# Kernel optimization log

Measured on AMD Instinct MI355X. Metric: run time of the kernel, lower is better.

Reference implementation:

```python
import jax, jax.numpy as jnp
import numpy as np

B, T, I, H = 256, 512, 300, 128


def setup_inputs() -> dict:
    key = jax.random.key(0)
    ks = jax.random.split(key, 7)
    s_ih = 1.0 / np.sqrt(H)
    return {
        "x": jax.random.normal(ks[0], (B, T, I), dtype=jnp.float32),
        # PyTorch LSTM params, gate order i,f,g,o stacked along first axis
        "W_ih": jax.random.uniform(ks[1], (4 * H, I), minval=-s_ih, maxval=s_ih, dtype=jnp.float32),
        "W_hh": jax.random.uniform(ks[2], (4 * H, H), minval=-s_ih, maxval=s_ih, dtype=jnp.float32),
        "b_ih": jax.random.uniform(ks[3], (4 * H,), minval=-s_ih, maxval=s_ih, dtype=jnp.float32),
        "b_hh": jax.random.uniform(ks[4], (4 * H,), minval=-s_ih, maxval=s_ih, dtype=jnp.float32),
        "fc_w": jax.random.uniform(ks[5], (1, H), minval=-s_ih, maxval=s_ih, dtype=jnp.float32),
        "fc_b": jax.random.uniform(ks[6], (1,), minval=-s_ih, maxval=s_ih, dtype=jnp.float32),
    }


def _lstm_last_h(x, W_ih, W_hh, b_ih, b_hh):
    # Precompute input contributions for all timesteps at once: [B,T,4H]
    xg = jnp.einsum("bti,gi->btg", x, W_ih) + b_ih + b_hh
    xg = jnp.transpose(xg, (1, 0, 2))  # [T,B,4H] for scan

    def step(carry, xg_t):
        h, c = carry
        gates = xg_t + h @ W_hh.T  # [B,4H]
        i, f, g, o = jnp.split(gates, 4, axis=-1)
        i = jax.nn.sigmoid(i)
        f = jax.nn.sigmoid(f)
        g = jnp.tanh(g)
        o = jax.nn.sigmoid(o)
        c = f * c + i * g
        h = o * jnp.tanh(c)
        return (h, c), None

    h0 = jnp.zeros((x.shape[0], W_hh.shape[1]), dtype=x.dtype)
    (h_last, _), _ = jax.lax.scan(step, (h0, h0), xg)
    return h_last  # [B,H]


def reference(x, W_ih, W_hh, b_ih, b_hh, fc_w, fc_b):
    h_last = _lstm_last_h(x, W_ih, W_hh, b_ih, b_hh)
    return h_last @ fc_w.T + fc_b  # [B,1]
```

## Files before the change

kernel.cpp:

```cpp
#include <hip/hip_runtime.h>
#include <cstdint>
#include <cstddef>

#define Bb   256
#define Tt   512
#define Ii   300
#define Hh   128
#define G4   512
#define KP   320
#define Mm   (Bb*Tt)

typedef _Float16 h2v   __attribute__((ext_vector_type(2)));
typedef _Float16 half8 __attribute__((ext_vector_type(8)));
typedef float    f32x4 __attribute__((ext_vector_type(4)));

static __device__ __forceinline__ h2v as_h2(unsigned int u){ union{unsigned int u; h2v h;} c; c.u=u; return c.h; }
static __device__ __forceinline__ unsigned int as_u32(h2v h){ union{unsigned int u; h2v h;} c; c.h=h; return c.u; }

#if __has_builtin(__builtin_amdgcn_fdot2)
#define FDOT2(a,b,c) __builtin_amdgcn_fdot2((a),(b),(c),false)
#else
static __device__ __forceinline__ float FDOT2(h2v a, h2v b, float c){
  return c + (float)a[0]*(float)b[0] + (float)a[1]*(float)b[1];
}
#endif

__global__ __launch_bounds__(256) void conv_x(const float* __restrict__ x, unsigned int* __restrict__ x16){
  int idx = blockIdx.x*256 + threadIdx.x;
  int r   = idx / 160;
  int kk2 = idx - r*160;
  int kk  = kk2*2;
  const float* xr = x + (size_t)r*Ii;
  float v0 = (kk   < Ii) ? xr[kk]   : 0.f;
  float v1 = (kk+1 < Ii) ? xr[kk+1] : 0.f;
  h2v h; h[0] = (_Float16)v0; h[1] = (_Float16)v1;
  x16[idx] = as_u32(h);
}

__global__ __launch_bounds__(256) void conv_small(const float* __restrict__ Wih, const float* __restrict__ Whh,
      const float* __restrict__ bih, const float* __restrict__ bhh,
      unsigned int* __restrict__ W16, unsigned int* __restrict__ Whh2, float* __restrict__ bias){
  int idx = blockIdx.x*256 + threadIdx.x;
  if (idx < G4*160){
    int pr = idx/160, kk2 = idx - pr*160, kk = kk2*2;
    int gc = (pr&3)*128 + (pr>>2);
    const float* wr = Wih + (size_t)gc*Ii;
    float v0 = (kk   < Ii) ? wr[kk]   : 0.f;
    float v1 = (kk+1 < Ii) ? wr[kk+1] : 0.f;
    h2v h; h[0]=(_Float16)v0; h[1]=(_Float16)v1;
    W16[idx] = as_u32(h);
  } else if (idx < G4*160 + G4*64){
    int t = idx - G4*160; int pr = t>>6, kk = t&63;
    int gc = (pr&3)*128 + (pr>>2);
    float v0 = Whh[gc*Hh + kk*2], v1 = Whh[gc*Hh + kk*2 + 1];
    h2v h; h[0]=(_Float16)v0; h[1]=(_Float16)v1;
    Whh2[t] = as_u32(h);
  } else if (idx < G4*160 + G4*64 + G4){
    int pr = idx - (G4*160 + G4*64);
    int gc = (pr&3)*128 + (pr>>2);
    bias[pr] = bih[gc] + bhh[gc];
  }
}

__global__ __launch_bounds__(256,2) void gemm16(const _Float16* __restrict__ A, const _Float16* __restrict__ Bm,
       const float* __restrict__ bias, float* __restrict__ C){
  __shared__ _Float16 As[128][32];
  __shared__ _Float16 Bs[128][32];
  int tid = threadIdx.x;
  int w = tid>>6, lane = tid&63;
  int bm = blockIdx.x*128, bn = blockIdx.y*128;
  f32x4 acc[2][8];
  #pragma unroll
  for (int i=0;i<2;i++)
    #pragma unroll
    for (int j=0;j<8;j++) acc[i][j] = (f32x4){0.f,0.f,0.f,0.f};

  int srow = tid>>1, scol = (tid&1)*16;
  const uint4* ga = (const uint4*)(A  + (size_t)(bm+srow)*KP + scol);
  const uint4* gb = (const uint4*)(Bm + (size_t)(bn+srow)*KP + scol);

  int q = lane>>4, mr = lane&15;
  int m0 = w*32;

  for (int kt=0; kt<KP/32; ++kt){
    __syncthreads();
    uint4 va0 = ga[0], va1 = ga[1];
    uint4 vb0 = gb[0], vb1 = gb[1];
    *(uint4*)&As[srow][scol]   = va0; *(uint4*)&As[srow][scol+8] = va1;
    *(uint4*)&Bs[srow][scol]   = vb0; *(uint4*)&Bs[srow][scol+8] = vb1;
    ga += 4; gb += 4;
    __syncthreads();
    half8 af0 = *(const half8*)&As[m0 + mr][q*8];
    half8 af1 = *(const half8*)&As[m0 + 16 + mr][q*8];
    #pragma unroll
    for (int j=0;j<8;j++){
      half8 bf = *(const half8*)&Bs[j*16 + mr][q*8];
      acc[0][j] = __builtin_amdgcn_mfma_f32_16x16x32_f16(af0, bf, acc[0][j], 0,0,0);
      acc[1][j] = __builtin_amdgcn_mfma_f32_16x16x32_f16(af1, bf, acc[1][j], 0,0,0);
    }
  }
  #pragma unroll
  for (int j=0;j<8;j++){
    int gc = bn + j*16 + mr;
    float bv = bias[gc];
    #pragma unroll
    for (int i=0;i<2;i++){
      int gr0 = bm + w*32 + i*16 + q*4;
      #pragma unroll
      for (int reg=0; reg<4; ++reg)
        C[(size_t)(gr0+reg)*G4 + gc] = acc[i][j][reg] + bv;
    }
  }
}

__global__ __launch_bounds__(512,1) void lstm_rec(const float* __restrict__ xg, const unsigned int* __restrict__ Whh2,
     const float* __restrict__ fcw, const float* __restrict__ fcb, float* __restrict__ out){
  int tid = threadIdx.x;
  int b = blockIdx.x;
  int d = tid >> 2, g = tid & 3;
  h2v w[64];
  #pragma unroll
  for (int kk=0; kk<64; ++kk) w[kk] = as_h2(Whh2[tid*64 + kk]);

  __shared__ __align__(16) unsigned short hsh[2][128];
  __shared__ float red[128];
  if (tid < 128) hsh[0][tid] = 0;
  float creg = 0.f, hreg = 0.f;
  const float* xrow = xg + (size_t)b * (Tt*G4);
  float xc = xrow[tid];
  int b0 = g & 1;
  int b1 = (g >> 1) & 1;
  float km = (g == 2) ? 2.f : 1.f;
  __syncthreads();

  for (int t=0; t<Tt; ++t){
    float xn = 0.f;
    if (t < Tt-1) xn = xrow[(size_t)(t+1)*G4 + tid];
    const uint4* hv = (const uint4*)hsh[t & 1];
    float a0 = xc, a1 = 0.f, a2 = 0.f, a3 = 0.f;
    #pragma unroll
    for (int kq=0; kq<8; ++kq){
      uint4 hq0 = hv[kq*2], hq1 = hv[kq*2+1];
      a0 = FDOT2(as_h2(hq0.x), w[kq*8+0], a0); a1 = FDOT2(as_h2(hq0.y), w[kq*8+1], a1);
      a2 = FDOT2(as_h2(hq0.z), w[kq*8+2], a2); a3 = FDOT2(as_h2(hq0.w), w[kq*8+3], a3);
      a0 = FDOT2(as_h2(hq1.x), w[kq*8+4], a0); a1 = FDOT2(as_h2(hq1.y), w[kq*8+5], a1);
      a2 = FDOT2(as_h2(hq1.z), w[kq*8+6], a2); a3 = FDOT2(as_h2(hq1.w), w[kq*8+7], a3);
    }
    float a = (a0 + a1) + (a2 + a3);
    float s  = 1.f/(1.f + __expf(-km*a));
    float act = (g == 2) ? (2.f*s - 1.f) : s;
    float u1 = __shfl_xor(act, 1);
    float u2 = __shfl_xor(act, 2);
    float u3 = __shfl_xor(act, 3);
    float pl = b0 ? u1  : act;
    float ph = b0 ? u3  : u2;
    float ql = b0 ? act : u1;
    float qh = b0 ? u2  : u3;
    float i_ = b1 ? ph : pl;
    float f_ = b1 ? qh : ql;
    float g_ = b1 ? pl : ph;
    float o_ = b1 ? ql : qh;
    creg = f_*creg + i_*g_;
    float ec = __expf(2.f*creg); float tc = 1.f - 2.f/(ec+1.f);
    hreg = o_*tc;
    if (g == 0){
      union{ _Float16 f; unsigned short s; } cv; cv.f = (_Float16)hreg;
      hsh[(t+1) & 1][d] = cv.s;
    }
    __syncthreads();
    xc = xn;
  }

  if (g == 0) red[d] = hreg * fcw[d];
  __syncthreads();
  #pragma unroll
  for (int s2=64; s2>=1; s2>>=1){
    if (tid < s2) red[tid] += red[tid+s2];
    __syncthreads();
  }
  if (tid == 0) out[b] = red[0] + fcb[0];
}

extern "C" void kernel_launch(void* const* d_in, const int* in_sizes, int n_in,
                              void* d_out, int out_size, void* d_ws, size_t ws_size,
                              hipStream_t stream){
  const float* x   = (const float*)d_in[0];
  const float* Wih = (const float*)d_in[1];
  const float* Whh = (const float*)d_in[2];
  const float* bih = (const float*)d_in[3];
  const float* bhh = (const float*)d_in[4];
  const float* fcw = (const float*)d_in[5];
  const float* fcb = (const float*)d_in[6];
  float* out = (float*)d_out;
  char* ws = (char*)d_ws;

  unsigned int* x16   = (unsigned int*)(ws);
  unsigned int* W16   = (unsigned int*)(ws + 83886080);
  unsigned int* Whh2w = (unsigned int*)(ws + 84213760);
  float*        bias  = (float*)      (ws + 84344832);
  float*        xg    = (float*)      (ws + 84346880);

  hipLaunchKernelGGL(conv_x,     dim3(81920),  dim3(256), 0, stream, x, x16);
  hipLaunchKernelGGL(conv_small, dim3(450),    dim3(256), 0, stream, Wih, Whh, bih, bhh, W16, Whh2w, bias);
  hipLaunchKernelGGL(gemm16,     dim3(1024,4), dim3(256), 0, stream,
                     (const _Float16*)x16, (const _Float16*)W16, bias, xg);
  hipLaunchKernelGGL(lstm_rec,   dim3(256),    dim3(512), 0, stream, xg, Whh2w, fcw, fcb, out);
}
```

Before: 638.9 us.

## Process two batch rows per LSTM block with DPP quad permutes and deeper prefetch

The recurrent kernel now handles two batch elements per workgroup, so each thread's W_hh fragment is reused for two dot products and the grid shrinks from 256 to 128 blocks. The two sequences run interleaved, which gives the per-step serial chain more independent work to hide latency. Cross-lane gate exchange uses DPP quad permutes instead of shfl_xor. xg is prefetched two steps ahead instead of one. In exchange only half the CUs are used, and each step does twice the LDS reads and math per thread.

```diff
diff --git a/kernel.cpp b/kernel.cpp
--- a/kernel.cpp
+++ b/kernel.cpp
@@ -24,6 +24,16 @@
   return c + (float)a[0]*(float)b[0] + (float)a[1]*(float)b[1];
 }
 #endif
+
+template<int CTRL>
+static __device__ __forceinline__ float qperm(float v){
+  union{float f; int i;} c; c.f = v;
+  c.i = __builtin_amdgcn_update_dpp(c.i, c.i, CTRL, 0xF, 0xF, false);
+  return c.f;
+}
+#define QP_XOR1 0xB1
+#define QP_XOR2 0x4E
+#define QP_XOR3 0x1B
 
 __global__ __launch_bounds__(256) void conv_x(const float* __restrict__ x, unsigned int* __restrict__ x16){
   int idx = blockIdx.x*256 + threadIdx.x;
@@ -116,69 +126,103 @@
 __global__ __launch_bounds__(512,1) void lstm_rec(const float* __restrict__ xg, const unsigned int* __restrict__ Whh2,
      const float* __restrict__ fcw, const float* __restrict__ fcb, float* __restrict__ out){
   int tid = threadIdx.x;
-  int b = blockIdx.x;
+  int b2 = blockIdx.x;
   int d = tid >> 2, g = tid & 3;
   h2v w[64];
   #pragma unroll
   for (int kk=0; kk<64; ++kk) w[kk] = as_h2(Whh2[tid*64 + kk]);
 
-  __shared__ __align__(16) unsigned short hsh[2][128];
-  __shared__ float red[128];
-  if (tid < 128) hsh[0][tid] = 0;
-  float creg = 0.f, hreg = 0.f;
-  const float* xrow = xg + (size_t)b * (Tt*G4);
-  float xc = xrow[tid];
-  int b0 = g & 1;
-  int b1 = (g >> 1) & 1;
+  __shared__ __align__(16) unsigned short hsh[2][2][128];
+  __shared__ float red[256];
+  if (tid < 256) ((unsigned short*)hsh)[tid] = 0;
+  float c0 = 0.f, h0 = 0.f, c1 = 0.f, h1 = 0.f;
+  const float* xrow0 = xg + (size_t)(2*b2)   * (Tt*G4);
+  const float* xrow1 = xg + (size_t)(2*b2+1) * (Tt*G4);
+  float xc0 = xrow0[tid],        xc1 = xrow1[tid];
+  float xa0 = xrow0[G4 + tid],   xa1 = xrow1[G4 + tid];
+  int b0m = g & 1;
+  int b1m = (g >> 1) & 1;
   float km = (g == 2) ? 2.f : 1.f;
   __syncthreads();
 
   for (int t=0; t<Tt; ++t){
-    float xn = 0.f;
-    if (t < Tt-1) xn = xrow[(size_t)(t+1)*G4 + tid];
-    const uint4* hv = (const uint4*)hsh[t & 1];
-    float a0 = xc, a1 = 0.f, a2 = 0.f, a3 = 0.f;
+    int tl = (t+2 < Tt) ? (t+2) : (Tt-1);
+    float xb0 = xrow0[(size_t)tl*G4 + tid];
+    float xb1 = xrow1[(size_t)tl*G4 + tid];
+
+    const uint4* hv0 = (const uint4*)hsh[t & 1][0];
+    const uint4* hv1 = (const uint4*)hsh[t & 1][1];
+    float p0 = xc0, p1 = 0.f, p2 = 0.f, p3 = 0.f;
+    float q0 = xc1, q1 = 0.f, q2 = 0.f, q3 = 0.f;
     #pragma unroll
     for (int kq=0; kq<8; ++kq){
-      uint4 hq0 = hv[kq*2], hq1 = hv[kq*2+1];
-      a0 = FDOT2(as_h2(hq0.x), w[kq*8+0], a0); a1 = FDOT2(as_h2(hq0.y), w[kq*8+1], a1);
-      a2 = FDOT2(as_h2(hq0.z), w[kq*8+2], a2); a3 = FDOT2(as_h2(hq0.w), w[kq*8+3], a3);
-      a0 = FDOT2(as_h2(hq1.x), w[kq*8+4], a0); a1 = FDOT2(as_h2(hq1.y), w[kq*8+5], a1);
-      a2 = FDOT2(as_h2(hq1.z), w[kq*8+6], a2); a3 = FDOT2(as_h2(hq1.w), w[kq*8+7], a3);
-    }
-    float a = (a0 + a1) + (a2 + a3);
-    float s  = 1.f/(1.f + __expf(-km*a));
-    float act = (g == 2) ? (2.f*s - 1.f) : s;
-    float u1 = __shfl_xor(act, 1);
-    float u2 = __shfl_xor(act, 2);
-    float u3 = __shfl_xor(act, 3);
-    float pl = b0 ? u1  : act;
-    float ph = b0 ? u3  : u2;
-    float ql = b0 ? act : u1;
-    float qh = b0 ? u2  : u3;
-    float i_ = b1 ? ph : pl;
-    float f_ = b1 ? qh : ql;
-    float g_ = b1 ? pl : ph;
-    float o_ = b1 ? ql : qh;
-    creg = f_*creg + i_*g_;
-    float ec = __expf(2.f*creg); float tc = 1.f - 2.f/(ec+1.f);
-    hreg = o_*tc;
+      uint4 ha = hv0[kq*2], hb = hv0[kq*2+1];
+      uint4 hc = hv1[kq*2], hd = hv1[kq*2+1];
+      p0 = FDOT2(as_h2(ha.x), w[kq*8+0], p0);
+      p1 = FDOT2(as_h2(ha.y), w[kq*8+1], p1);
+      p2 = FDOT2(as_h2(ha.z), w[kq*8+2], p2);
+      p3 = FDOT2(as_h2(ha.w), w[kq*8+3], p3);
+      q0 = FDOT2(as_h2(hc.x), w[kq*8+0], q0);
+      q1 = FDOT2(as_h2(hc.y), w[kq*8+1], q1);
+      q2 = FDOT2(as_h2(hc.z), w[kq*8+2], q2);
+      q3 = FDOT2(as_h2(hc.w), w[kq*8+3], q3);
+      p0 = FDOT2(as_h2(hb.x), w[kq*8+4], p0);
+      p1 = FDOT2(as_h2(hb.y), w[kq*8+5], p1);
+      p2 = FDOT2(as_h2(hb.z), w[kq*8+6], p2);
+      p3 = FDOT2(as_h2(hb.w), w[kq*8+7], p3);
+      q0 = FDOT2(as_h2(hd.x), w[kq*8+4], q0);
+      q1 = FDOT2(as_h2(hd.y), w[kq*8+5], q1);
+      q2 = FDOT2(as_h2(hd.z), w[kq*8+6], q2);
+      q3 = FDOT2(as_h2(hd.w), w[kq*8+7], q3);
+    }
+    float aA = (p0 + p1) + (p2 + p3);
+    float aB = (q0 + q1) + (q2 + q3);
+    float sA  = 1.f/(1.f + __expf(-km*aA));
+    float sB  = 1.f/(1.f + __expf(-km*aB));
+    float actA = (g == 2) ? (2.f*sA - 1.f) : sA;
+    float actB = (g == 2) ? (2.f*sB - 1.f) : sB;
+    float uA1 = qperm<QP_XOR1>(actA), uA2 = qperm<QP_XOR2>(actA), uA3 = qperm<QP_XOR3>(actA);
+    float uB1 = qperm<QP_XOR1>(actB), uB2 = qperm<QP_XOR2>(actB), uB3 = qperm<QP_XOR3>(actB);
+    {
+      float pl = b0m ? uA1  : actA, ph = b0m ? uA3 : uA2;
+      float ql = b0m ? actA : uA1,  qh = b0m ? uA2 : uA3;
+      float i_ = b1m ? ph : pl, f_ = b1m ? qh : ql;
+      float g_ = b1m ? pl : ph, o_ = b1m ? ql : qh;
+      c0 = f_*c0 + i_*g_;
+      float ec = __expf(2.f*c0); float tc = 1.f - 2.f/(ec+1.f);
+      h0 = o_*tc;
+    }
+    {
+      float pl = b0m ? uB1  : actB, ph = b0m ? uB3 : uB2;
+      float ql = b0m ? actB : uB1,  qh = b0m ? uB2 : uB3;
+      float i_ = b1m ? ph : pl, f_ = b1m ? qh : ql;
+      float g_ = b1m ? pl : ph, o_ = b1m ? ql : qh;
+      c1 = f_*c1 + i_*g_;
+      float ec = __expf(2.f*c1); float tc = 1.f - 2.f/(ec+1.f);
+      h1 = o_*tc;
+    }
     if (g == 0){
-      union{ _Float16 f; unsigned short s; } cv; cv.f = (_Float16)hreg;
-      hsh[(t+1) & 1][d] = cv.s;
-    }
-    __syncthreads();
-    xc = xn;
-  }
-
-  if (g == 0) red[d] = hreg * fcw[d];
+      union{ _Float16 f; unsigned short s; } cv; cv.f = (_Float16)h0;
+      hsh[(t+1) & 1][0][d] = cv.s;
+    } else if (g == 1){
+      union{ _Float16 f; unsigned short s; } cv; cv.f = (_Float16)h1;
+      hsh[(t+1) & 1][1][d] = cv.s;
+    }
+    __syncthreads();
+    xc0 = xa0; xa0 = xb0;
+    xc1 = xa1; xa1 = xb1;
+  }
+
+  if (g == 0) red[d]       = h0 * fcw[d];
+  else if (g == 1) red[128 + d] = h1 * fcw[d];
   __syncthreads();
   #pragma unroll
   for (int s2=64; s2>=1; s2>>=1){
-    if (tid < s2) red[tid] += red[tid+s2];
-    __syncthreads();
-  }
-  if (tid == 0) out[b] = red[0] + fcb[0];
+    if ((tid & 127) < s2 && tid < 256) red[tid] += red[tid+s2];
+    __syncthreads();
+  }
+  if (tid == 0)   out[2*b2]   = red[0]   + fcb[0];
+  if (tid == 128) out[2*b2+1] = red[128] + fcb[0];
 }
 
 extern "C" void kernel_launch(void* const* d_in, const int* in_sizes, int n_in,
@@ -204,5 +248,5 @@
   hipLaunchKernelGGL(conv_small, dim3(450),    dim3(256), 0, stream, Wih, Whh, bih, bhh, W16, Whh2w, bias);
   hipLaunchKernelGGL(gemm16,     dim3(1024,4), dim3(256), 0, stream,
                      (const _Float16*)x16, (const _Float16*)W16, bias, xg);
-  hipLaunchKernelGGL(lstm_rec,   dim3(256),    dim3(512), 0, stream, xg, Whh2w, fcw, fcb, out);
-}
+  hipLaunchKernelGGL(lstm_rec,   dim3(128),    dim3(512), 0, stream, xg, Whh2w, fcw, fcb, out);
+}
```

After: 923.2 us. +44.5%, slower.

## Split LSTM recurrent dot products across thread pairs with DPP lane exchange

Applied to the files above, without the earlier changes.

Doubles the recurrent kernel's block size to 1024 threads so each gate row's 128-wide dot product is split between two threads holding 32 weight pairs each, halving per-thread serial FDOT2 work and register usage. Partial sums are combined and gate activations exchanged with DPP quad permutes instead of ds_swizzle-based shuffles. The xg prefetch is deepened to two steps ahead. The trade-off is more waves participating in each per-step __syncthreads barrier and duplicated activation math across thread pairs.

```diff
diff --git a/kernel.cpp b/kernel.cpp
--- a/kernel.cpp
+++ b/kernel.cpp
@@ -24,6 +24,17 @@
   return c + (float)a[0]*(float)b[0] + (float)a[1]*(float)b[1];
 }
 #endif
+
+template<int CTRL>
+static __device__ __forceinline__ float qperm(float v){
+  union{float f; int i;} c; c.f = v;
+  c.i = __builtin_amdgcn_update_dpp(c.i, c.i, CTRL, 0xF, 0xF, false);
+  return c.f;
+}
+#define QP_XOR1   0xB1
+#define QP_XOR2   0x4E
+#define QP_XOR3   0x1B
+#define ROW_HMIRR 0x141
 
 __global__ __launch_bounds__(256) void conv_x(const float* __restrict__ x, unsigned int* __restrict__ x16){
   int idx = blockIdx.x*256 + threadIdx.x;
@@ -49,14 +60,17 @@
     float v1 = (kk+1 < Ii) ? wr[kk+1] : 0.f;
     h2v h; h[0]=(_Float16)v0; h[1]=(_Float16)v1;
     W16[idx] = as_u32(h);
-  } else if (idx < G4*160 + G4*64){
-    int t = idx - G4*160; int pr = t>>6, kk = t&63;
+  } else if (idx < G4*160 + 1024*32){
+    int t = idx - G4*160;
+    int thrd = t >> 5, j = t & 31;
+    int pr = thrd >> 1, kh = thrd & 1;
     int gc = (pr&3)*128 + (pr>>2);
+    int kk = kh*32 + j;
     float v0 = Whh[gc*Hh + kk*2], v1 = Whh[gc*Hh + kk*2 + 1];
     h2v h; h[0]=(_Float16)v0; h[1]=(_Float16)v1;
     Whh2[t] = as_u32(h);
-  } else if (idx < G4*160 + G4*64 + G4){
-    int pr = idx - (G4*160 + G4*64);
+  } else if (idx < G4*160 + 1024*32 + G4){
+    int pr = idx - (G4*160 + 1024*32);
     int gc = (pr&3)*128 + (pr>>2);
     bias[pr] = bih[gc] + bhh[gc];
   }
@@ -113,65 +127,73 @@
   }
 }
 
-__global__ __launch_bounds__(512,1) void lstm_rec(const float* __restrict__ xg, const unsigned int* __restrict__ Whh2,
+__global__ __launch_bounds__(1024) void lstm_rec(const float* __restrict__ xg, const unsigned int* __restrict__ Whh2,
      const float* __restrict__ fcw, const float* __restrict__ fcb, float* __restrict__ out){
   int tid = threadIdx.x;
   int b = blockIdx.x;
-  int d = tid >> 2, g = tid & 3;
-  h2v w[64];
-  #pragma unroll
-  for (int kk=0; kk<64; ++kk) w[kk] = as_h2(Whh2[tid*64 + kk]);
+  int pr = tid >> 1, kh = tid & 1;
+  int g = pr & 3;
+  h2v w[32];
+  #pragma unroll
+  for (int j=0; j<32; ++j) w[j] = as_h2(Whh2[tid*32 + j]);
 
   __shared__ __align__(16) unsigned short hsh[2][128];
   __shared__ float red[128];
   if (tid < 128) hsh[0][tid] = 0;
   float creg = 0.f, hreg = 0.f;
   const float* xrow = xg + (size_t)b * (Tt*G4);
-  float xc = xrow[tid];
-  int b0 = g & 1;
-  int b1 = (g >> 1) & 1;
+  float xc = xrow[pr];
+  float xa = xrow[G4 + pr];
+  int b0m = g & 1;
+  int b1m = (g >> 1) & 1;
   float km = (g == 2) ? 2.f : 1.f;
   __syncthreads();
 
   for (int t=0; t<Tt; ++t){
-    float xn = 0.f;
-    if (t < Tt-1) xn = xrow[(size_t)(t+1)*G4 + tid];
-    const uint4* hv = (const uint4*)hsh[t & 1];
-    float a0 = xc, a1 = 0.f, a2 = 0.f, a3 = 0.f;
-    #pragma unroll
-    for (int kq=0; kq<8; ++kq){
-      uint4 hq0 = hv[kq*2], hq1 = hv[kq*2+1];
-      a0 = FDOT2(as_h2(hq0.x), w[kq*8+0], a0); a1 = FDOT2(as_h2(hq0.y), w[kq*8+1], a1);
-      a2 = FDOT2(as_h2(hq0.z), w[kq*8+2], a2); a3 = FDOT2(as_h2(hq0.w), w[kq*8+3], a3);
-      a0 = FDOT2(as_h2(hq1.x), w[kq*8+4], a0); a1 = FDOT2(as_h2(hq1.y), w[kq*8+5], a1);
-      a2 = FDOT2(as_h2(hq1.z), w[kq*8+6], a2); a3 = FDOT2(as_h2(hq1.w), w[kq*8+7], a3);
-    }
-    float a = (a0 + a1) + (a2 + a3);
+    int tl = (t+2 < Tt) ? (t+2) : (Tt-1);
+    float xb = xrow[(size_t)tl*G4 + pr];
+
+    const uint4* hv = (const uint4*)hsh[t & 1] + kh*8;
+    float p0 = kh ? 0.f : xc, p1 = 0.f, p2 = 0.f, p3 = 0.f;
+    #pragma unroll
+    for (int kq=0; kq<4; ++kq){
+      uint4 ha = hv[kq*2], hb = hv[kq*2+1];
+      p0 = FDOT2(as_h2(ha.x), w[kq*8+0], p0);
+      p1 = FDOT2(as_h2(ha.y), w[kq*8+1], p1);
+      p2 = FDOT2(as_h2(ha.z), w[kq*8+2], p2);
+      p3 = FDOT2(as_h2(ha.w), w[kq*8+3], p3);
+      p0 = FDOT2(as_h2(hb.x), w[kq*8+4], p0);
+      p1 = FDOT2(as_h2(hb.y), w[kq*8+5], p1);
+      p2 = FDOT2(as_h2(hb.z), w[kq*8+6], p2);
+      p3 = FDOT2(as_h2(hb.w), w[kq*8+7], p3);
+    }
+    float a = (p0 + p1) + (p2 + p3);
+    a += qperm<QP_XOR1>(a);
     float s  = 1.f/(1.f + __expf(-km*a));
     float act = (g == 2) ? (2.f*s - 1.f) : s;
-    float u1 = __shfl_xor(act, 1);
-    float u2 = __shfl_xor(act, 2);
-    float u3 = __shfl_xor(act, 3);
-    float pl = b0 ? u1  : act;
-    float ph = b0 ? u3  : u2;
-    float ql = b0 ? act : u1;
-    float qh = b0 ? u2  : u3;
-    float i_ = b1 ? ph : pl;
-    float f_ = b1 ? qh : ql;
-    float g_ = b1 ? pl : ph;
-    float o_ = b1 ? ql : qh;
+    float A1 = qperm<QP_XOR2>(act);
+    float A3 = qperm<ROW_HMIRR>(act);
+    float A2 = qperm<QP_XOR3>(A3);
+    float pl = b0m ? A1  : act;
+    float ph = b0m ? A3  : A2;
+    float ql = b0m ? act : A1;
+    float qh = b0m ? A2  : A3;
+    float i_ = b1m ? ph : pl;
+    float f_ = b1m ? qh : ql;
+    float g_ = b1m ? pl : ph;
+    float o_ = b1m ? ql : qh;
     creg = f_*creg + i_*g_;
     float ec = __expf(2.f*creg); float tc = 1.f - 2.f/(ec+1.f);
     hreg = o_*tc;
-    if (g == 0){
+    if ((tid & 7) == 0){
       union{ _Float16 f; unsigned short s; } cv; cv.f = (_Float16)hreg;
-      hsh[(t+1) & 1][d] = cv.s;
-    }
-    __syncthreads();
-    xc = xn;
-  }
-
-  if (g == 0) red[d] = hreg * fcw[d];
+      hsh[(t+1) & 1][tid >> 3] = cv.s;
+    }
+    __syncthreads();
+    xc = xa; xa = xb;
+  }
+
+  if ((tid & 7) == 0) red[tid >> 3] = hreg * fcw[tid >> 3];
   __syncthreads();
   #pragma unroll
   for (int s2=64; s2>=1; s2>>=1){
@@ -204,5 +226,5 @@
   hipLaunchKernelGGL(conv_small, dim3(450),    dim3(256), 0, stream, Wih, Whh, bih, bhh, W16, Whh2w, bias);
   hipLaunchKernelGGL(gemm16,     dim3(1024,4), dim3(256), 0, stream,
                      (const _Float16*)x16, (const _Float16*)W16, bias, xg);
-  hipLaunchKernelGGL(lstm_rec,   dim3(256),    dim3(512), 0, stream, xg, Whh2w, fcw, fcb, out);
-}
+  hipLaunchKernelGGL(lstm_rec,   dim3(256),    dim3(1024), 0, stream, xg, Whh2w, fcw, fcb, out);
+}
```

After: 765.3 us. 19.8% more time.

## Fuse fp32-to-fp16 input conversion into GEMM and prefetch deeper in recurrence

Applied to the files above, without the earlier changes.

Drops the separate conv_x pass. The GEMM now loads fp32 x directly with float4 loads, converts it to fp16 in registers and prefetches the next K tile into registers before the MMA phase. This removes a full write and re-read of a half-precision copy of x, at the cost of each GEMM column block re-reading the larger fp32 input. The LSTM recurrence now prefetches the input gates two timesteps ahead and replaces the quad shuffles with DPP quad_perm moves to shorten the per-step critical path.

```diff
diff --git a/kernel.cpp b/kernel.cpp
--- a/kernel.cpp
+++ b/kernel.cpp
@@ -25,17 +25,15 @@
 }
 #endif
 
-__global__ __launch_bounds__(256) void conv_x(const float* __restrict__ x, unsigned int* __restrict__ x16){
-  int idx = blockIdx.x*256 + threadIdx.x;
-  int r   = idx / 160;
-  int kk2 = idx - r*160;
-  int kk  = kk2*2;
-  const float* xr = x + (size_t)r*Ii;
-  float v0 = (kk   < Ii) ? xr[kk]   : 0.f;
-  float v1 = (kk+1 < Ii) ? xr[kk+1] : 0.f;
-  h2v h; h[0] = (_Float16)v0; h[1] = (_Float16)v1;
-  x16[idx] = as_u32(h);
-}
+template<int CTRL>
+static __device__ __forceinline__ float qperm(float v){
+  union{float f; int i;} c; c.f = v;
+  c.i = __builtin_amdgcn_update_dpp(c.i, c.i, CTRL, 0xF, 0xF, false);
+  return c.f;
+}
+#define QP_XOR1 0xB1
+#define QP_XOR2 0x4E
+#define QP_XOR3 0x1B
 
 __global__ __launch_bounds__(256) void conv_small(const float* __restrict__ Wih, const float* __restrict__ Whh,
       const float* __restrict__ bih, const float* __restrict__ bhh,
@@ -62,7 +60,7 @@
   }
 }
 
-__global__ __launch_bounds__(256,2) void gemm16(const _Float16* __restrict__ A, const _Float16* __restrict__ Bm,
+__global__ __launch_bounds__(256,2) void gemm16(const float* __restrict__ X, const _Float16* __restrict__ Bm,
        const float* __restrict__ bias, float* __restrict__ C){
   __shared__ _Float16 As[128][32];
   __shared__ _Float16 Bs[128][32];
@@ -76,19 +74,49 @@
     for (int j=0;j<8;j++) acc[i][j] = (f32x4){0.f,0.f,0.f,0.f};
 
   int srow = tid>>1, scol = (tid&1)*16;
-  const uint4* ga = (const uint4*)(A  + (size_t)(bm+srow)*KP + scol);
-  const uint4* gb = (const uint4*)(Bm + (size_t)(bn+srow)*KP + scol);
+  const float*    xr = X  + (size_t)(bm+srow)*Ii;
+  const _Float16* br = Bm + (size_t)(bn+srow)*KP;
 
   int q = lane>>4, mr = lane&15;
   int m0 = w*32;
 
+  float4 a4[4];
+  uint4  b4[2];
+  {
+    #pragma unroll
+    for (int i=0;i<4;i++){
+      int c = scol + i*4;
+      a4[i] = (c <= Ii-4) ? *(const float4*)(xr + c) : (float4){0.f,0.f,0.f,0.f};
+    }
+    b4[0] = *(const uint4*)(br + scol);
+    b4[1] = *(const uint4*)(br + scol + 8);
+  }
+
   for (int kt=0; kt<KP/32; ++kt){
     __syncthreads();
-    uint4 va0 = ga[0], va1 = ga[1];
-    uint4 vb0 = gb[0], vb1 = gb[1];
-    *(uint4*)&As[srow][scol]   = va0; *(uint4*)&As[srow][scol+8] = va1;
-    *(uint4*)&Bs[srow][scol]   = vb0; *(uint4*)&Bs[srow][scol+8] = vb1;
-    ga += 4; gb += 4;
+    union { _Float16 h[16]; uint4 u[2]; } ah;
+    #pragma unroll
+    for (int i=0;i<4;i++){
+      ah.h[i*4+0] = (_Float16)a4[i].x;
+      ah.h[i*4+1] = (_Float16)a4[i].y;
+      ah.h[i*4+2] = (_Float16)a4[i].z;
+      ah.h[i*4+3] = (_Float16)a4[i].w;
+    }
+    *(uint4*)&As[srow][scol]   = ah.u[0];
+    *(uint4*)&As[srow][scol+8] = ah.u[1];
+    *(uint4*)&Bs[srow][scol]   = b4[0];
+    *(uint4*)&Bs[srow][scol+8] = b4[1];
+    if (kt+1 < KP/32){
+      int c0 = (kt+1)*32 + scol;
+      #pragma unroll
+      for (int i=0;i<4;i++){
+        int c = c0 + i*4;
+        a4[i] = (c <= Ii-4) ? *(const float4*)(xr + c) : (float4){0.f,0.f,0.f,0.f};
+      }
+      const _Float16* bb = br + (kt+1)*32;
+      b4[0] = *(const uint4*)(bb + scol);
+      b4[1] = *(const uint4*)(bb + scol + 8);
+    }
     __syncthreads();
     half8 af0 = *(const half8*)&As[m0 + mr][q*8];
     half8 af1 = *(const half8*)&As[m0 + 16 + mr][q*8];
@@ -128,14 +156,16 @@
   float creg = 0.f, hreg = 0.f;
   const float* xrow = xg + (size_t)b * (Tt*G4);
   float xc = xrow[tid];
+  float xa = xrow[G4 + tid];
   int b0 = g & 1;
   int b1 = (g >> 1) & 1;
   float km = (g == 2) ? 2.f : 1.f;
   __syncthreads();
 
   for (int t=0; t<Tt; ++t){
-    float xn = 0.f;
-    if (t < Tt-1) xn = xrow[(size_t)(t+1)*G4 + tid];
+    int tl = (t+2 < Tt) ? (t+2) : (Tt-1);
+    float xb = xrow[(size_t)tl*G4 + tid];
+
     const uint4* hv = (const uint4*)hsh[t & 1];
     float a0 = xc, a1 = 0.f, a2 = 0.f, a3 = 0.f;
     #pragma unroll
@@ -149,9 +179,9 @@
     float a = (a0 + a1) + (a2 + a3);
     float s  = 1.f/(1.f + __expf(-km*a));
     float act = (g == 2) ? (2.f*s - 1.f) : s;
-    float u1 = __shfl_xor(act, 1);
-    float u2 = __shfl_xor(act, 2);
-    float u3 = __shfl_xor(act, 3);
+    float u1 = qperm<QP_XOR1>(act);
+    float u2 = qperm<QP_XOR2>(act);
+    float u3 = qperm<QP_XOR3>(act);
     float pl = b0 ? u1  : act;
     float ph = b0 ? u3  : u2;
     float ql = b0 ? act : u1;
@@ -168,7 +198,7 @@
       hsh[(t+1) & 1][d] = cv.s;
     }
     __syncthreads();
-    xc = xn;
+    xc = xa; xa = xb;
   }
 
   if (g == 0) red[d] = hreg * fcw[d];
@@ -194,15 +224,13 @@
   float* out = (float*)d_out;
   char* ws = (char*)d_ws;
 
-  unsigned int* x16   = (unsigned int*)(ws);
   unsigned int* W16   = (unsigned int*)(ws + 83886080);
   unsigned int* Whh2w = (unsigned int*)(ws + 84213760);
   float*        bias  = (float*)      (ws + 84344832);
   float*        xg    = (float*)      (ws + 84346880);
 
-  hipLaunchKernelGGL(conv_x,     dim3(81920),  dim3(256), 0, stream, x, x16);
   hipLaunchKernelGGL(conv_small, dim3(450),    dim3(256), 0, stream, Wih, Whh, bih, bhh, W16, Whh2w, bias);
   hipLaunchKernelGGL(gemm16,     dim3(1024,4), dim3(256), 0, stream,
-                     (const _Float16*)x16, (const _Float16*)W16, bias, xg);
+                     x, (const _Float16*)W16, bias, xg);
   hipLaunchKernelGGL(lstm_rec,   dim3(256),    dim3(512), 0, stream, xg, Whh2w, fcw, fcb, out);
 }
```

Measured after the change: 884.8 us. 38.5% more time.
